# Performance work log

Measured on AMD Instinct MI355X. Metric: run time of the kernel, lower is better.

Reference implementation:

```python
import jax, jax.numpy as jnp
import numpy as np

B, S, D, UNITS = 64, 2048, 1024, 1024


def setup_inputs() -> dict:
    key = jax.random.key(0)
    ks = jax.random.split(key, 5)
    sc = 1.0 / np.sqrt(D)
    return {
        "s_prev": jax.random.normal(ks[0], (B, D), jnp.float32),
        "hidden_states": jax.random.normal(ks[1], (B, S, D), jnp.float32),
        "W_kernel": jax.random.normal(ks[2], (D, UNITS), jnp.float32) * sc,
        "W_bias": jnp.zeros((UNITS,), jnp.float32),
        "U_kernel": jax.random.normal(ks[3], (D, UNITS), jnp.float32) * sc,
        "U_bias": jnp.zeros((UNITS,), jnp.float32),
        "V_kernel": jax.random.normal(ks[4], (UNITS, 1), jnp.float32) * (1.0 / np.sqrt(UNITS)),
        "V_bias": jnp.zeros((1,), jnp.float32),
    }


def reference(s_prev, hidden_states, W_kernel, W_bias, U_kernel, U_bias, V_kernel, V_bias):
    # W(s_prev): [B, units], broadcast over seq axis
    w_s = (s_prev @ W_kernel + W_bias)[:, None, :]          # [B, 1, units]
    u_h = jnp.einsum('bsd,du->bsu', hidden_states, U_kernel) + U_bias  # [B, S, units]
    scores = jnp.tanh(w_s + u_h) @ V_kernel + V_bias        # [B, S, 1]
    weight = jax.nn.softmax(scores, axis=1)                 # [B, S, 1]
    context = jnp.sum(hidden_states * weight, axis=1)       # [B, D]
    return (context, weight)
```

## Files before the change

kernel.cpp:

```cpp
#include <hip/hip_runtime.h>
#include <stdint.h>

#define NB 64
#define NS 2048
#define ND 1024
#define NU 1024

typedef __attribute__((ext_vector_type(8))) _Float16 f16x8;
typedef __attribute__((ext_vector_type(4))) _Float16 f16x4;
typedef __attribute__((ext_vector_type(4))) float f32x4;

__device__ __forceinline__ void gload_lds16(const void* g, void* l) {
    __builtin_amdgcn_global_load_lds(
        (const __attribute__((address_space(1))) unsigned int*)g,
        (__attribute__((address_space(3))) unsigned int*)l, 16, 0, 0);
}

__global__ void convert_h(const float* __restrict__ h, _Float16* __restrict__ hf, size_t n8) {
    size_t i = (size_t)blockIdx.x * blockDim.x + threadIdx.x;
    size_t stride = (size_t)gridDim.x * blockDim.x;
    for (; i < n8; i += stride) {
        const float4* p = (const float4*)(h + i * 8);
        float4 a = p[0], b = p[1];
        union { _Float16 e[8]; uint4 v; } o;
        o.e[0] = (_Float16)a.x; o.e[1] = (_Float16)a.y;
        o.e[2] = (_Float16)a.z; o.e[3] = (_Float16)a.w;
        o.e[4] = (_Float16)b.x; o.e[5] = (_Float16)b.y;
        o.e[6] = (_Float16)b.z; o.e[7] = (_Float16)b.w;
        *(uint4*)(hf + i * 8) = o.v;
    }
}

__global__ void transpose_u(const float* __restrict__ Uk, _Float16* __restrict__ Ut) {
    __shared__ float tile[64][65];
    int d0 = blockIdx.x * 64, u0 = blockIdx.y * 64;
    int tid = threadIdx.x;
    #pragma unroll
    for (int i = 0; i < 16; ++i) {
        int idx = i * 256 + tid;
        int r = idx >> 6, c = idx & 63;
        tile[r][c] = Uk[(size_t)(d0 + r) * NU + (u0 + c)];
    }
    __syncthreads();
    #pragma unroll
    for (int i = 0; i < 16; ++i) {
        int idx = i * 256 + tid;
        int c = idx >> 6, r = idx & 63;
        Ut[(size_t)(u0 + c) * ND + (d0 + r)] = (_Float16)tile[r][c];
    }
}

__global__ void prep_off(const float* __restrict__ s_prev, const float* __restrict__ Wk,
                         const float* __restrict__ Wb, const float* __restrict__ Ub,
                         float* __restrict__ off) {
    int blk = blockIdx.x;
    int b = blk >> 2, ut = blk & 3;
    int tid = threadIdx.x;
    int u = ut * 256 + tid;
    __shared__ float sp[ND];
    #pragma unroll
    for (int i = tid; i < ND; i += 256) sp[i] = s_prev[(size_t)b * ND + i];
    __syncthreads();
    float acc = 0.f;
    #pragma unroll 8
    for (int d = 0; d < ND; ++d) acc += sp[d] * Wk[(size_t)d * NU + u];
    off[(size_t)b * NU + u] = acc + Wb[u] + Ub[u];
}

__launch_bounds__(256, 4)
__global__ void scores_f16(const _Float16* __restrict__ hf,
                           const _Float16* __restrict__ Ut,
                           const float* __restrict__ off,
                           const float* __restrict__ V,
                           float* __restrict__ scores)
{
    int hw = blockIdx.x;
    int chunk = gridDim.x >> 3;
    int logical = (hw & 7) * chunk + (hw >> 3);
    int ublk = logical & 7;
    int t2 = logical >> 3;
    int sblk = t2 & 15;
    int b = t2 >> 4;
    int s0 = sblk * 128, u0 = ublk * 128;

    __shared__ _Float16 As[128][32];
    __shared__ _Float16 Bs[128][32];

    int tid = threadIdx.x;
    int w = tid >> 6, l = tid & 63;
    int wr = w >> 1, wc = w & 1;
    int rg = l >> 4, cl = l & 15;

    f32x4 acc[4][4] = {};

    const _Float16* srcA[2];
    const _Float16* srcB[2];
    #pragma unroll
    for (int i = 0; i < 2; ++i) {
        int row = w * 32 + i * 16 + (l >> 2);
        int gs = ((l & 3) ^ ((row >> 1) & 3)) * 8;
        srcA[i] = hf + ((size_t)b * NS + s0 + row) * ND + gs;
        srcB[i] = Ut + (size_t)(u0 + row) * ND + gs;
    }

    for (int kk = 0; kk < 32; ++kk) {
        int k0 = kk * 32;
        __syncthreads();
        #pragma unroll
        for (int i = 0; i < 2; ++i) {
            gload_lds16((const void*)(srcA[i] + k0), (void*)&As[w * 32 + i * 16][0]);
            gload_lds16((const void*)(srcB[i] + k0), (void*)&Bs[w * 32 + i * 16][0]);
        }
        __syncthreads();

        f16x8 af[4], bf[4];
        #pragma unroll
        for (int m = 0; m < 4; ++m) {
            int r_ = wr * 64 + m * 16 + cl;
            af[m] = *(const f16x8*)&As[r_][(rg ^ ((r_ >> 1) & 3)) * 8];
        }
        #pragma unroll
        for (int n = 0; n < 4; ++n) {
            int r_ = wc * 64 + n * 16 + cl;
            bf[n] = *(const f16x8*)&Bs[r_][(rg ^ ((r_ >> 1) & 3)) * 8];
        }
        #pragma unroll
        for (int m = 0; m < 4; ++m)
            #pragma unroll
            for (int n = 0; n < 4; ++n)
                acc[m][n] = __builtin_amdgcn_mfma_f32_16x16x32_f16(af[m], bf[n], acc[m][n], 0, 0, 0);
    }

    float offv[4], vv[4];
    #pragma unroll
    for (int n = 0; n < 4; ++n) {
        int u = u0 + wc * 64 + n * 16 + cl;
        offv[n] = off[(size_t)b * NU + u];
        vv[n] = V[u];
    }
    #pragma unroll
    for (int m = 0; m < 4; ++m) {
        #pragma unroll
        for (int i = 0; i < 4; ++i) {
            float sacc = 0.f;
            #pragma unroll
            for (int n = 0; n < 4; ++n) {
                float x = acc[m][n][i] + offv[n];
                float t = 1.0f - 2.0f / (1.0f + __expf(2.0f * x));
                sacc += t * vv[n];
            }
            #pragma unroll
            for (int msk = 1; msk < 16; msk <<= 1) sacc += __shfl_xor(sacc, msk, 64);
            if (cl == 0)
                atomicAdd(&scores[(size_t)b * NS + s0 + wr * 64 + m * 16 + rg * 4 + i], sacc);
        }
    }
}

__launch_bounds__(256, 4)
__global__ void scores_kernel(const float* __restrict__ h,
                              const _Float16* __restrict__ Ut,
                              const float* __restrict__ off,
                              const float* __restrict__ V,
                              float* __restrict__ scores)
{
    int hw = blockIdx.x;
    int chunk = gridDim.x >> 3;
    int logical = (hw & 7) * chunk + (hw >> 3);
    int ublk = logical & 7;
    int t2 = logical >> 3;
    int sblk = t2 & 15;
    int b = t2 >> 4;
    int s0 = sblk * 128, u0 = ublk * 128;

    __shared__ _Float16 As[2][128][32];
    __shared__ _Float16 Bs[3][128][32];

    int tid = threadIdx.x;
    int w = tid >> 6, l = tid & 63;
    int wr = w >> 1, wc = w & 1;
    int rg = l >> 4, cl = l & 15;

    f32x4 acc[4][4] = {};

    const float* hA = h + ((size_t)b * NS + s0) * ND;
    int arow = tid >> 3;
    int acol4 = (tid & 7) * 4;
    int aslog = (tid & 7) >> 1;
    int ahalf = tid & 1;
    const _Float16* srcB[2];
    #pragma unroll
    for (int i = 0; i < 2; ++i) {
        int row = w * 32 + i * 16 + (l >> 2);
        srcB[i] = Ut + (size_t)(u0 + row) * ND + (((l & 3) ^ ((row >> 1) & 3)) * 8);
    }

    float4 av[4];

    #define LOADA(KK) { \
        _Pragma("unroll") \
        for (int p = 0; p < 4; ++p) \
            av[p] = *(const float4*)(hA + (size_t)(p * 32 + arow) * ND + (KK) * 32 + acol4); \
    }
    #define ISSUEB(BI, KK) { \
        _Pragma("unroll") \
        for (int i = 0; i < 2; ++i) \
            gload_lds16((const void*)(srcB[i] + (KK) * 32), (void*)&Bs[BI][w * 32 + i * 16][0]); \
    }
    #define CVTW(ABUF) { \
        _Pragma("unroll") \
        for (int p = 0; p < 4; ++p) { \
            int r_ = p * 32 + arow; \
            int sp_ = aslog ^ ((r_ >> 1) & 3); \
            union { _Float16 e[4]; uint2 u2; } cv; \
            cv.e[0] = (_Float16)av[p].x; cv.e[1] = (_Float16)av[p].y; \
            cv.e[2] = (_Float16)av[p].z; cv.e[3] = (_Float16)av[p].w; \
            *(uint2*)&As[ABUF][r_][sp_ * 8 + ahalf * 4] = cv.u2; \
        } \
    }
    #define COMPUTE(ABUF, BI) { \
        f16x8 af[4], bf[4]; \
        _Pragma("unroll") \
        for (int m = 0; m < 4; ++m) { \
            int r_ = wr * 64 + m * 16 + cl; \
            af[m] = *(const f16x8*)&As[ABUF][r_][(rg ^ ((r_ >> 1) & 3)) * 8]; \
        } \
        _Pragma("unroll") \
        for (int n = 0; n < 4; ++n) { \
            int r_ = wc * 64 + n * 16 + cl; \
            bf[n] = *(const f16x8*)&Bs[BI][r_][(rg ^ ((r_ >> 1) & 3)) * 8]; \
        } \
        _Pragma("unroll") \
        for (int m = 0; m < 4; ++m) \
            _Pragma("unroll") \
            for (int n = 0; n < 4; ++n) \
                acc[m][n] = __builtin_amdgcn_mfma_f32_16x16x32_f16(af[m], bf[n], acc[m][n], 0, 0, 0); \
    }

    LOADA(0);
    ISSUEB(0, 0);
    int bcur = 0;
    for (int t = 0; t < 31; ++t) {
        asm volatile("s_waitcnt vmcnt(2)" ::: "memory");
        __builtin_amdgcn_sched_barrier(0);
        CVTW(t & 1);
        LOADA(t + 1);
        int bnxt = bcur + 1; if (bnxt == 3) bnxt = 0;
        ISSUEB(bnxt, t + 1);
        asm volatile("s_waitcnt vmcnt(6) lgkmcnt(0)" ::: "memory");
        __builtin_amdgcn_sched_barrier(0);
        __builtin_amdgcn_s_barrier();
        __builtin_amdgcn_sched_barrier(0);
        COMPUTE(t & 1, bcur);
        bcur = bnxt;
    }
    asm volatile("s_waitcnt vmcnt(0)" ::: "memory");
    __builtin_amdgcn_sched_barrier(0);
    CVTW(1);
    asm volatile("s_waitcnt lgkmcnt(0)" ::: "memory");
    __builtin_amdgcn_sched_barrier(0);
    __builtin_amdgcn_s_barrier();
    __builtin_amdgcn_sched_barrier(0);
    COMPUTE(1, bcur);

    #undef LOADA
    #undef ISSUEB
    #undef CVTW
    #undef COMPUTE

    float offv[4], vv[4];
    #pragma unroll
    for (int n = 0; n < 4; ++n) {
        int u = u0 + wc * 64 + n * 16 + cl;
        offv[n] = off[(size_t)b * NU + u];
        vv[n] = V[u];
    }
    #pragma unroll
    for (int m = 0; m < 4; ++m) {
        #pragma unroll
        for (int i = 0; i < 4; ++i) {
            float sacc = 0.f;
            #pragma unroll
            for (int n = 0; n < 4; ++n) {
                float x = acc[m][n][i] + offv[n];
                float t = 1.0f - 2.0f / (1.0f + __expf(2.0f * x));
                sacc += t * vv[n];
            }
            #pragma unroll
            for (int msk = 1; msk < 16; msk <<= 1) sacc += __shfl_xor(sacc, msk, 64);
            if (cl == 0)
                atomicAdd(&scores[(size_t)b * NS + s0 + wr * 64 + m * 16 + rg * 4 + i], sacc);
        }
    }
}

__global__ void softmax_kernel(const float* __restrict__ scores, float* __restrict__ outw) {
    int b = blockIdx.x, tid = threadIdx.x;
    const float* src = scores + (size_t)b * NS;
    float4 x0 = *(const float4*)(src + tid * 8);
    float4 x1 = *(const float4*)(src + tid * 8 + 4);
    float m = fmaxf(fmaxf(fmaxf(x0.x, x0.y), fmaxf(x0.z, x0.w)),
                    fmaxf(fmaxf(x1.x, x1.y), fmaxf(x1.z, x1.w)));
    #pragma unroll
    for (int msk = 1; msk < 64; msk <<= 1) m = fmaxf(m, __shfl_xor(m, msk, 64));
    __shared__ float redm[4], reds[4];
    if ((tid & 63) == 0) redm[tid >> 6] = m;
    __syncthreads();
    m = fmaxf(fmaxf(redm[0], redm[1]), fmaxf(redm[2], redm[3]));
    float e[8];
    e[0] = __expf(x0.x - m); e[1] = __expf(x0.y - m); e[2] = __expf(x0.z - m); e[3] = __expf(x0.w - m);
    e[4] = __expf(x1.x - m); e[5] = __expf(x1.y - m); e[6] = __expf(x1.z - m); e[7] = __expf(x1.w - m);
    float s = e[0] + e[1] + e[2] + e[3] + e[4] + e[5] + e[6] + e[7];
    #pragma unroll
    for (int msk = 1; msk < 64; msk <<= 1) s += __shfl_xor(s, msk, 64);
    if ((tid & 63) == 0) reds[tid >> 6] = s;
    __syncthreads();
    float Z = reds[0] + reds[1] + reds[2] + reds[3];
    float r = 1.0f / Z;
    float4 o0 = { e[0] * r, e[1] * r, e[2] * r, e[3] * r };
    float4 o1 = { e[4] * r, e[5] * r, e[6] * r, e[7] * r };
    *(float4*)(outw + (size_t)b * NS + tid * 8) = o0;
    *(float4*)(outw + (size_t)b * NS + tid * 8 + 4) = o1;
}

__global__ void context_partial_f16(const _Float16* __restrict__ hf, const float* __restrict__ wgt,
                                    float* __restrict__ part) {
    int sc = blockIdx.x, b = blockIdx.y, tid = threadIdx.x;
    __shared__ float lw[128];
    if (tid < 128) lw[tid] = wgt[(size_t)b * NS + sc * 128 + tid];
    __syncthreads();
    const _Float16* hb = hf + ((size_t)b * NS + sc * 128) * ND + tid * 4;
    float4 acc = { 0.f, 0.f, 0.f, 0.f };
    #pragma unroll 4
    for (int s = 0; s < 128; ++s) {
        f16x4 hv = *(const f16x4*)(hb + (size_t)s * ND);
        float wv = lw[s];
        acc.x += (float)hv[0] * wv; acc.y += (float)hv[1] * wv;
        acc.z += (float)hv[2] * wv; acc.w += (float)hv[3] * wv;
    }
    *(float4*)(part + ((size_t)(sc * NB + b)) * ND + tid * 4) = acc;
}

__global__ void context_partial(const float* __restrict__ h, const float* __restrict__ wgt,
                                float* __restrict__ part) {
    int sc = blockIdx.x, b = blockIdx.y, tid = threadIdx.x;
    __shared__ float lw[128];
    if (tid < 128) lw[tid] = wgt[(size_t)b * NS + sc * 128 + tid];
    __syncthreads();
    const float* hb = h + ((size_t)b * NS + sc * 128) * ND + tid * 4;
    float4 acc = { 0.f, 0.f, 0.f, 0.f };
    #pragma unroll 4
    for (int s = 0; s < 128; ++s) {
        float4 hv = *(const float4*)(hb + (size_t)s * ND);
        float wv = lw[s];
        acc.x += hv.x * wv; acc.y += hv.y * wv; acc.z += hv.z * wv; acc.w += hv.w * wv;
    }
    *(float4*)(part + ((size_t)(sc * NB + b)) * ND + tid * 4) = acc;
}

__global__ void context_reduce(const float* __restrict__ part, float* __restrict__ outc) {
    int b = blockIdx.x, tid = threadIdx.x;
    float4 acc = { 0.f, 0.f, 0.f, 0.f };
    #pragma unroll
    for (int k = 0; k < 16; ++k) {
        float4 p = *(const float4*)(part + ((size_t)(k * NB + b)) * ND + tid * 4);
        acc.x += p.x; acc.y += p.y; acc.z += p.z; acc.w += p.w;
    }
    *(float4*)(outc + (size_t)b * ND + tid * 4) = acc;
}

extern "C" void kernel_launch(void* const* d_in, const int* in_sizes, int n_in,
                              void* d_out, int out_size, void* d_ws, size_t ws_size,
                              hipStream_t stream) {
    const float* s_prev = (const float*)d_in[0];
    const float* hidden = (const float*)d_in[1];
    const float* Wk     = (const float*)d_in[2];
    const float* Wb     = (const float*)d_in[3];
    const float* Uk     = (const float*)d_in[4];
    const float* Ub     = (const float*)d_in[5];
    const float* Vk     = (const float*)d_in[6];

    float* out_ctx = (float*)d_out;
    float* out_w   = out_ctx + NB * ND;

    char* ws = (char*)d_ws;
    _Float16* Ut  = (_Float16*)ws;
    float* off    = (float*)(ws + (size_t)(2 << 20));
    float* scores = (float*)(ws + (size_t)(2 << 20) + (256 << 10));
    float* part   = (float*)(ws + (size_t)(2 << 20) + (768 << 10));
    size_t small  = (size_t)(2 << 20) + (768 << 10) + (4 << 20);
    _Float16* hf16 = (_Float16*)(ws + small);
    size_t hbytes = (size_t)NB * NS * ND * sizeof(_Float16);

    bool fast = (ws_size >= small + hbytes);

    hipMemsetAsync(scores, 0, (size_t)NB * NS * sizeof(float), stream);
    transpose_u<<<dim3(16, 16), 256, 0, stream>>>(Uk, Ut);
    prep_off<<<256, 256, 0, stream>>>(s_prev, Wk, Wb, Ub, off);

    if (fast) {
        size_t n8 = (size_t)NB * NS * ND / 8;
        convert_h<<<8192, 256, 0, stream>>>(hidden, hf16, n8);
        scores_f16<<<8192, 256, 0, stream>>>(hf16, Ut, off, Vk, scores);
        softmax_kernel<<<NB, 256, 0, stream>>>(scores, out_w);
        context_partial_f16<<<dim3(16, NB), 256, 0, stream>>>(hf16, out_w, part);
    } else {
        scores_kernel<<<8192, 256, 0, stream>>>(hidden, Ut, off, Vk, scores);
        softmax_kernel<<<NB, 256, 0, stream>>>(scores, out_w);
        context_partial<<<dim3(16, NB), 256, 0, stream>>>(hidden, out_w, part);
    }
    context_reduce<<<NB, 256, 0, stream>>>(part, out_ctx);
}
```

Measured before the change: 610.4 us.

## Replace f16 scores GEMM with 256x256-tile, 512-thread, triple-buffered pipelined kernel

Replaces the fp16 scores kernel, which used 128x128 tiles with two syncthreads per k-step and no prefetch, with a 256x256-tile kernel. It runs 8 waves per block, triple-buffers async global-to-LDS loads so loads for step k+2 overlap the MFMAs for step k, and raises wave priority around the MFMA block. The larger tile halves how often each operand is reloaded from global memory and the pipeline hides load latency. In exchange it needs more registers (128 accumulator floats per lane) and 96KB of LDS per block, which lowers occupancy, and it launches fewer blocks (2048). The fp32 fallback kernel is only moved within the file.

```diff
diff --git a/kernel.cpp b/kernel.cpp
--- a/kernel.cpp
+++ b/kernel.cpp
@@ -67,12 +67,133 @@
     off[(size_t)b * NU + u] = acc + Wb[u] + Ub[u];
 }
 
-__launch_bounds__(256, 4)
-__global__ void scores_f16(const _Float16* __restrict__ hf,
+__launch_bounds__(512, 2)
+__global__ void scores_big(const _Float16* __restrict__ hf,
                            const _Float16* __restrict__ Ut,
                            const float* __restrict__ off,
                            const float* __restrict__ V,
                            float* __restrict__ scores)
+{
+    int hw = blockIdx.x;
+    int chunk = gridDim.x >> 3;
+    int logical = (hw & 7) * chunk + (hw >> 3);
+    int ublk = logical & 3;
+    int t2 = logical >> 2;
+    int sblk = t2 & 7;
+    int b = t2 >> 3;
+    int s0 = sblk * 256, u0 = ublk * 256;
+
+    __shared__ _Float16 As[3][256][32];
+    __shared__ _Float16 Bs[3][256][32];
+
+    int tid = threadIdx.x;
+    int w = tid >> 6, l = tid & 63;
+    int wr = w >> 2, wc = w & 3;
+    int rg = l >> 4, cl = l & 15;
+
+    f32x4 acc[8][4] = {};
+
+    const _Float16* srcA[2];
+    const _Float16* srcB[2];
+    #pragma unroll
+    for (int i = 0; i < 2; ++i) {
+        int row = w * 32 + i * 16 + (l >> 2);
+        int gs = ((l & 3) ^ ((row >> 1) & 3)) * 8;
+        srcA[i] = hf + ((size_t)b * NS + s0 + row) * ND + gs;
+        srcB[i] = Ut + (size_t)(u0 + row) * ND + gs;
+    }
+
+    #define STAGE(BUF, KK) { \
+        _Pragma("unroll") \
+        for (int i = 0; i < 2; ++i) { \
+            gload_lds16((const void*)(srcA[i] + (KK) * 32), (void*)&As[BUF][w * 32 + i * 16][0]); \
+            gload_lds16((const void*)(srcB[i] + (KK) * 32), (void*)&Bs[BUF][w * 32 + i * 16][0]); \
+        } \
+    }
+
+    #define COMPUTE(BUF) { \
+        f16x8 af[8], bf[4]; \
+        _Pragma("unroll") \
+        for (int m = 0; m < 8; ++m) { \
+            int r_ = wr * 128 + m * 16 + cl; \
+            af[m] = *(const f16x8*)&As[BUF][r_][(rg ^ ((r_ >> 1) & 3)) * 8]; \
+        } \
+        _Pragma("unroll") \
+        for (int n = 0; n < 4; ++n) { \
+            int r_ = wc * 64 + n * 16 + cl; \
+            bf[n] = *(const f16x8*)&Bs[BUF][r_][(rg ^ ((r_ >> 1) & 3)) * 8]; \
+        } \
+        __builtin_amdgcn_s_setprio(1); \
+        _Pragma("unroll") \
+        for (int m = 0; m < 8; ++m) \
+            _Pragma("unroll") \
+            for (int n = 0; n < 4; ++n) \
+                acc[m][n] = __builtin_amdgcn_mfma_f32_16x16x32_f16(af[m], bf[n], acc[m][n], 0, 0, 0); \
+        __builtin_amdgcn_s_setprio(0); \
+    }
+
+    STAGE(0, 0);
+    STAGE(1, 1);
+
+    int bi = 0;
+    for (int t = 0; t < 30; ++t) {
+        asm volatile("s_waitcnt vmcnt(4)" ::: "memory");
+        __builtin_amdgcn_sched_barrier(0);
+        __builtin_amdgcn_s_barrier();
+        __builtin_amdgcn_sched_barrier(0);
+        int bn = bi + 2; if (bn >= 3) bn -= 3;
+        STAGE(bn, t + 2);
+        __builtin_amdgcn_sched_barrier(0);
+        COMPUTE(bi);
+        ++bi; if (bi == 3) bi = 0;
+    }
+    asm volatile("s_waitcnt vmcnt(4)" ::: "memory");
+    __builtin_amdgcn_sched_barrier(0);
+    __builtin_amdgcn_s_barrier();
+    __builtin_amdgcn_sched_barrier(0);
+    COMPUTE(bi);
+    ++bi; if (bi == 3) bi = 0;
+    asm volatile("s_waitcnt vmcnt(0)" ::: "memory");
+    __builtin_amdgcn_sched_barrier(0);
+    __builtin_amdgcn_s_barrier();
+    __builtin_amdgcn_sched_barrier(0);
+    COMPUTE(bi);
+
+    #undef STAGE
+    #undef COMPUTE
+
+    float offv[4], vv[4];
+    #pragma unroll
+    for (int n = 0; n < 4; ++n) {
+        int u = u0 + wc * 64 + n * 16 + cl;
+        offv[n] = off[(size_t)b * NU + u];
+        vv[n] = V[u];
+    }
+    #pragma unroll
+    for (int m = 0; m < 8; ++m) {
+        #pragma unroll
+        for (int i = 0; i < 4; ++i) {
+            float sacc = 0.f;
+            #pragma unroll
+            for (int n = 0; n < 4; ++n) {
+                float x = acc[m][n][i] + offv[n];
+                float t = 1.0f - 2.0f / (1.0f + __expf(2.0f * x));
+                sacc += t * vv[n];
+            }
+            #pragma unroll
+            for (int msk = 1; msk < 16; msk <<= 1) sacc += __shfl_xor(sacc, msk, 64);
+            if (cl == 0)
+                atomicAdd(&scores[(size_t)b * NS + s0 + wr * 128 + m * 16 + rg * 4 + i], sacc);
+        }
+    }
+}
+
+__launch_bounds__(256, 4)
+__global__ void scores_kernel(const float* __restrict__ h,
+                              const _Float16* __restrict__ Ut,
+                              const float* __restrict__ off,
+                              const float* __restrict__ V,
+                              float* __restrict__ scores)
 {
     int hw = blockIdx.x;
     int chunk = gridDim.x >> 3;
@@ -83,8 +204,8 @@
     int b = t2 >> 4;
     int s0 = sblk * 128, u0 = ublk * 128;
 
-    __shared__ _Float16 As[128][32];
-    __shared__ _Float16 Bs[128][32];
+    __shared__ _Float16 As[2][128][32];
+    __shared__ _Float16 Bs[3][128][32];
 
     int tid = threadIdx.x;
     int w = tid >> 6, l = tid & 63;
@@ -93,43 +214,90 @@
 
     f32x4 acc[4][4] = {};
 
-    const _Float16* srcA[2];
+    const float* hA = h + ((size_t)b * NS + s0) * ND;
+    int arow = tid >> 3;
+    int acol4 = (tid & 7) * 4;
+    int aslog = (tid & 7) >> 1;
+    int ahalf = tid & 1;
     const _Float16* srcB[2];
     #pragma unroll
     for (int i = 0; i < 2; ++i) {
         int row = w * 32 + i * 16 + (l >> 2);
-        int gs = ((l & 3) ^ ((row >> 1) & 3)) * 8;
-        srcA[i] = hf + ((size_t)b * NS + s0 + row) * ND + gs;
-        srcB[i] = Ut + (size_t)(u0 + row) * ND + gs;
-    }
-
-    for (int kk = 0; kk < 32; ++kk) {
-        int k0 = kk * 32;
-        __syncthreads();
-        #pragma unroll
-        for (int i = 0; i < 2; ++i) {
-            gload_lds16((const void*)(srcA[i] + k0), (void*)&As[w * 32 + i * 16][0]);
-            gload_lds16((const void*)(srcB[i] + k0), (void*)&Bs[w * 32 + i * 16][0]);
-        }
-        __syncthreads();
-
-        f16x8 af[4], bf[4];
-        #pragma unroll
-        for (int m = 0; m < 4; ++m) {
-            int r_ = wr * 64 + m * 16 + cl;
-            af[m] = *(const f16x8*)&As[r_][(rg ^ ((r_ >> 1) & 3)) * 8];
-        }
-        #pragma unroll
-        for (int n = 0; n < 4; ++n) {
-            int r_ = wc * 64 + n * 16 + cl;
-            bf[n] = *(const f16x8*)&Bs[r_][(rg ^ ((r_ >> 1) & 3)) * 8];
-        }
-        #pragma unroll
-        for (int m = 0; m < 4; ++m)
-            #pragma unroll
-            for (int n = 0; n < 4; ++n)
-                acc[m][n] = __builtin_amdgcn_mfma_f32_16x16x32_f16(af[m], bf[n], acc[m][n], 0, 0, 0);
-    }
+        srcB[i] = Ut + (size_t)(u0 + row) * ND + (((l & 3) ^ ((row >> 1) & 3)) * 8);
+    }
+
+    float4 av[4];
+
+    #define LOADA(KK) { \
+        _Pragma("unroll") \
+        for (int p = 0; p < 4; ++p) \
+            av[p] = *(const float4*)(hA + (size_t)(p * 32 + arow) * ND + (KK) * 32 + acol4); \
+    }
+    #define ISSUEB(BI, KK) { \
+        _Pragma("unroll") \
+        for (int i = 0; i < 2; ++i) \
+            gload_lds16((const void*)(srcB[i] + (KK) * 32), (void*)&Bs[BI][w * 32 + i * 16][0]); \
+    }
+    #define CVTW(ABUF) { \
+        _Pragma("unroll") \
+        for (int p = 0; p < 4; ++p) { \
+            int r_ = p * 32 + arow; \
+            int sp_ = aslog ^ ((r_ >> 1) & 3); \
+            union { _Float16 e[4]; uint2 u2; } cv; \
+            cv.e[0] = (_Float16)av[p].x; cv.e[1] = (_Float16)av[p].y; \
+            cv.e[2] = (_Float16)av[p].z; cv.e[3] = (_Float16)av[p].w; \
+            *(uint2*)&As[ABUF][r_][sp_ * 8 + ahalf * 4] = cv.u2; \
+        } \
+    }
+    #define COMPUTE(ABUF, BI) { \
+        f16x8 af[4], bf[4]; \
+        _Pragma("unroll") \
+        for (int m = 0; m < 4; ++m) { \
+            int r_ = wr * 64 + m * 16 + cl; \
+            af[m] = *(const f16x8*)&As[ABUF][r_][(rg ^ ((r_ >> 1) & 3)) * 8]; \
+        } \
+        _Pragma("unroll") \
+        for (int n = 0; n < 4; ++n) { \
+            int r_ = wc * 64 + n * 16 + cl; \
+            bf[n] = *(const f16x8*)&Bs[BI][r_][(rg ^ ((r_ >> 1) & 3)) * 8]; \
+        } \
+        _Pragma("unroll") \
+        for (int m = 0; m < 4; ++m) \
+            _Pragma("unroll") \
+            for (int n = 0; n < 4; ++n) \
+                acc[m][n] = __builtin_amdgcn_mfma_f32_16x16x32_f16(af[m], bf[n], acc[m][n], 0, 0, 0); \
+    }
+
+    LOADA(0);
+    ISSUEB(0, 0);
+    int bcur = 0;
+    for (int t = 0; t < 31; ++t) {
+        asm volatile("s_waitcnt vmcnt(2)" ::: "memory");
+        __builtin_amdgcn_sched_barrier(0);
+        CVTW(t & 1);
+        LOADA(t + 1);
+        int bnxt = bcur + 1; if (bnxt == 3) bnxt = 0;
+        ISSUEB(bnxt, t + 1);
+        asm volatile("s_waitcnt vmcnt(6) lgkmcnt(0)" ::: "memory");
+        __builtin_amdgcn_sched_barrier(0);
+        __builtin_amdgcn_s_barrier();
+        __builtin_amdgcn_sched_barrier(0);
+        COMPUTE(t & 1, bcur);
+        bcur = bnxt;
+    }
+    asm volatile("s_waitcnt vmcnt(0)" ::: "memory");
+    __builtin_amdgcn_sched_barrier(0);
+    CVTW(1);
+    asm volatile("s_waitcnt lgkmcnt(0)" ::: "memory");
+    __builtin_amdgcn_sched_barrier(0);
+    __builtin_amdgcn_s_barrier();
+    __builtin_amdgcn_sched_barrier(0);
+    COMPUTE(1, bcur);
+
+    #undef LOADA
+    #undef ISSUEB
+    #undef CVTW
+    #undef COMPUTE
 
     float offv[4], vv[4];
     #pragma unroll
@@ -157,143 +325,6 @@
     }
 }
 
-__launch_bounds__(256, 4)
-__global__ void scores_kernel(const float* __restrict__ h,
-                              const _Float16* __restrict__ Ut,
-                              const float* __restrict__ off,
-                              const float* __restrict__ V,
-                              float* __restrict__ scores)
-{
-    int hw = blockIdx.x;
-    int chunk = gridDim.x >> 3;
-    int logical = (hw & 7) * chunk + (hw >> 3);
-    int ublk = logical & 7;
-    int t2 = logical >> 3;
-    int sblk = t2 & 15;
-    int b = t2 >> 4;
-    int s0 = sblk * 128, u0 = ublk * 128;
-
-    __shared__ _Float16 As[2][128][32];
-    __shared__ _Float16 Bs[3][128][32];
-
-    int tid = threadIdx.x;
-    int w = tid >> 6, l = tid & 63;
-    int wr = w >> 1, wc = w & 1;
-    int rg = l >> 4, cl = l & 15;
-
-    f32x4 acc[4][4] = {};
-
-    const float* hA = h + ((size_t)b * NS + s0) * ND;
-    int arow = tid >> 3;
-    int acol4 = (tid & 7) * 4;
-    int aslog = (tid & 7) >> 1;
-    int ahalf = tid & 1;
-    const _Float16* srcB[2];
-    #pragma unroll
-    for (int i = 0; i < 2; ++i) {
-        int row = w * 32 + i * 16 + (l >> 2);
-        srcB[i] = Ut + (size_t)(u0 + row) * ND + (((l & 3) ^ ((row >> 1) & 3)) * 8);
-    }
-
-    float4 av[4];
-
-    #define LOADA(KK) { \
-        _Pragma("unroll") \
-        for (int p = 0; p < 4; ++p) \
-            av[p] = *(const float4*)(hA + (size_t)(p * 32 + arow) * ND + (KK) * 32 + acol4); \
-    }
-    #define ISSUEB(BI, KK) { \
-        _Pragma("unroll") \
-        for (int i = 0; i < 2; ++i) \
-            gload_lds16((const void*)(srcB[i] + (KK) * 32), (void*)&Bs[BI][w * 32 + i * 16][0]); \
-    }
-    #define CVTW(ABUF) { \
-        _Pragma("unroll") \
-        for (int p = 0; p < 4; ++p) { \
-            int r_ = p * 32 + arow; \
-            int sp_ = aslog ^ ((r_ >> 1) & 3); \
-            union { _Float16 e[4]; uint2 u2; } cv; \
-            cv.e[0] = (_Float16)av[p].x; cv.e[1] = (_Float16)av[p].y; \
-            cv.e[2] = (_Float16)av[p].z; cv.e[3] = (_Float16)av[p].w; \
-            *(uint2*)&As[ABUF][r_][sp_ * 8 + ahalf * 4] = cv.u2; \
-        } \
-    }
-    #define COMPUTE(ABUF, BI) { \
-        f16x8 af[4], bf[4]; \
-        _Pragma("unroll") \
-        for (int m = 0; m < 4; ++m) { \
-            int r_ = wr * 64 + m * 16 + cl; \
-            af[m] = *(const f16x8*)&As[ABUF][r_][(rg ^ ((r_ >> 1) & 3)) * 8]; \
-        } \
-        _Pragma("unroll") \
-        for (int n = 0; n < 4; ++n) { \
-            int r_ = wc * 64 + n * 16 + cl; \
-            bf[n] = *(const f16x8*)&Bs[BI][r_][(rg ^ ((r_ >> 1) & 3)) * 8]; \
-        } \
-        _Pragma("unroll") \
-        for (int m = 0; m < 4; ++m) \
-            _Pragma("unroll") \
-            for (int n = 0; n < 4; ++n) \
-                acc[m][n] = __builtin_amdgcn_mfma_f32_16x16x32_f16(af[m], bf[n], acc[m][n], 0, 0, 0); \
-    }
-
-    LOADA(0);
-    ISSUEB(0, 0);
-    int bcur = 0;
-    for (int t = 0; t < 31; ++t) {
-        asm volatile("s_waitcnt vmcnt(2)" ::: "memory");
-        __builtin_amdgcn_sched_barrier(0);
-        CVTW(t & 1);
-        LOADA(t + 1);
-        int bnxt = bcur + 1; if (bnxt == 3) bnxt = 0;
-        ISSUEB(bnxt, t + 1);
-        asm volatile("s_waitcnt vmcnt(6) lgkmcnt(0)" ::: "memory");
-        __builtin_amdgcn_sched_barrier(0);
-        __builtin_amdgcn_s_barrier();
-        __builtin_amdgcn_sched_barrier(0);
-        COMPUTE(t & 1, bcur);
-        bcur = bnxt;
-    }
-    asm volatile("s_waitcnt vmcnt(0)" ::: "memory");
-    __builtin_amdgcn_sched_barrier(0);
-    CVTW(1);
-    asm volatile("s_waitcnt lgkmcnt(0)" ::: "memory");
-    __builtin_amdgcn_sched_barrier(0);
-    __builtin_amdgcn_s_barrier();
-    __builtin_amdgcn_sched_barrier(0);
-    COMPUTE(1, bcur);
-
-    #undef LOADA
-    #undef ISSUEB
-    #undef CVTW
-    #undef COMPUTE
-
-    float offv[4], vv[4];
-    #pragma unroll
-    for (int n = 0; n < 4; ++n) {
-        int u = u0 + wc * 64 + n * 16 + cl;
-        offv[n] = off[(size_t)b * NU + u];
-        vv[n] = V[u];
-    }
-    #pragma unroll
-    for (int m = 0; m < 4; ++m) {
-        #pragma unroll
-        for (int i = 0; i < 4; ++i) {
-            float sacc = 0.f;
-            #pragma unroll
-            for (int n = 0; n < 4; ++n) {
-                float x = acc[m][n][i] + offv[n];
-                float t = 1.0f - 2.0f / (1.0f + __expf(2.0f * x));
-                sacc += t * vv[n];
-            }
-            #pragma unroll
-            for (int msk = 1; msk < 16; msk <<= 1) sacc += __shfl_xor(sacc, msk, 64);
-            if (cl == 0)
-                atomicAdd(&scores[(size_t)b * NS + s0 + wr * 64 + m * 16 + rg * 4 + i], sacc);
-        }
-    }
-}
-
 __global__ void softmax_kernel(const float* __restrict__ scores, float* __restrict__ outw) {
     int b = blockIdx.x, tid = threadIdx.x;
     const float* src = scores + (size_t)b * NS;
@@ -401,7 +432,7 @@
     if (fast) {
         size_t n8 = (size_t)NB * NS * ND / 8;
         convert_h<<<8192, 256, 0, stream>>>(hidden, hf16, n8);
-        scores_f16<<<8192, 256, 0, stream>>>(hf16, Ut, off, Vk, scores);
+        scores_big<<<2048, 512, 0, stream>>>(hf16, Ut, off, Vk, scores);
         softmax_kernel<<<NB, 256, 0, stream>>>(scores, out_w);
         context_partial_f16<<<dim3(16, NB), 256, 0, stream>>>(hf16, out_w, part);
     } else {
```

Measured after the change: 684.2 us. +12.1%, slower.
